# Performance work log

Hardware: AMD Instinct MI355X
Metric: run time of the kernel (lower is better)

The kernel has to match this reference:

```python
import jax, jax.numpy as jnp
import numpy as np

B, T, C, H = 2, 2048, 1024, 16
D = C // H
CURV = 1.0  # clamp_curvature(1.0) -> 1.0
EPS = 1e-5


def layer_norm(x, w, b):
    mu = jnp.mean(x, axis=-1, keepdims=True)
    var = jnp.var(x, axis=-1, keepdims=True)
    return (x - mu) * jax.lax.rsqrt(var + EPS) * w + b


def mobius_addition(x, y, c):
    xn2 = jnp.sum(x * x, axis=-1, keepdims=True)
    yn2 = jnp.sum(y * y, axis=-1, keepdims=True)
    ip = jnp.sum(x * y, axis=-1, keepdims=True)
    num = (1 + 2 * c * ip + c * yn2) * x + (1 - c * xn2) * y
    den = 1 + 2 * c * ip + (c ** 2) * xn2 * yn2
    return num / den


def scaling_factor(x, c):
    xn2 = jnp.sum(x * x, axis=-1, keepdims=True)
    return 2.0 / (1.0 + c * xn2)


def expmap(x, v, c):
    lam = scaling_factor(x, c)
    vn = jnp.linalg.norm(v, axis=-1, keepdims=True)
    second = (1.0 / c ** 0.5) * jnp.tanh(jnp.sqrt(c * lam * vn ** 2 / 2.0)) * v / vn
    return mobius_addition(x, second, c)


def logmap(x, u, c):
    lam = scaling_factor(x, c)
    m = mobius_addition(-x, u, c)
    mn = jnp.linalg.norm(m, axis=-1, keepdims=True)
    cf = 2.0 / (lam * c ** 0.5)
    arg = jnp.clip(jnp.sqrt(c * mn), -0.999, 0.999)
    return cf * jnp.arctanh(arg) * m / mn


def calc_reference_point(x):
    # shift-right by one token, zero at position 0
    return jnp.pad(x[:, :-1, :], ((0, 0), (1, 0), (0, 0)))


def causal_attention(q, k, v):
    # q,k,v: [B,H,T,D]
    scores = jnp.einsum('bhqd,bhkd->bhqk', q, k) / np.sqrt(D).astype(np.float32)
    mask = jnp.tril(jnp.ones((T, T), dtype=bool))
    scores = jnp.where(mask, scores, -jnp.inf)
    att = jax.nn.softmax(scores, axis=-1)
    return jnp.einsum('bhqk,bhkd->bhqd', att, v)


def setup_inputs() -> dict:
    key = jax.random.key(0)
    ks = jax.random.split(key, 6)
    s = 0.02
    return {
        'x': jax.random.normal(ks[0], (B, T, C), jnp.float32),
        'ln1_w': jnp.ones((C,), jnp.float32),
        'ln1_b': jnp.zeros((C,), jnp.float32),
        'W_attn': jax.random.normal(ks[1], (C, 3 * C), jnp.float32) * s,
        'b_attn': jnp.zeros((3 * C,), jnp.float32),
        'W_aproj': jax.random.normal(ks[2], (C, C), jnp.float32) * s,
        'b_aproj': jnp.zeros((C,), jnp.float32),
        'ln2_w': jnp.ones((C,), jnp.float32),
        'ln2_b': jnp.zeros((C,), jnp.float32),
        'W_fc': jax.random.normal(ks[3], (C, 4 * C), jnp.float32) * s,
        'b_fc': jnp.zeros((4 * C,), jnp.float32),
        'W_mproj': jax.random.normal(ks[4], (4 * C, C), jnp.float32) * s,
        'b_mproj': jnp.zeros((C,), jnp.float32),
    }


def reference(x, ln1_w, ln1_b, W_attn, b_attn, W_aproj, b_aproj,
              ln2_w, ln2_b, W_fc, b_fc, W_mproj, b_mproj):
    c = CURV
    # --- attention branch ---
    xn = layer_norm(x, ln1_w, ln1_b)
    ref = calc_reference_point(xn)
    xt = logmap(ref, xn, c)
    qkv = xt @ W_attn + b_attn
    q, k, v = jnp.split(qkv, 3, axis=-1)
    q = q.reshape(B, T, H, D).transpose(0, 2, 1, 3)
    k = k.reshape(B, T, H, D).transpose(0, 2, 1, 3)
    v = v.reshape(B, T, H, D).transpose(0, 2, 1, 3)
    y = causal_attention(q, k, v)
    y = y.transpose(0, 2, 1, 3).reshape(B, T, C)
    y = expmap(ref, y, c)  # map_back_after_attention=True
    y = y @ W_aproj + b_aproj
    x = x + y
    # --- MLP branch (no expmap since map_back_after_attention) ---
    h = layer_norm(x, ln2_w, ln2_b)
    h = jax.nn.gelu(h @ W_fc + b_fc, approximate=False)
    h = h @ W_mproj + b_mproj
    return x + h
```

## Files before the change

kernel.cpp:

```cpp
#include <hip/hip_runtime.h>
#include <hip/hip_bf16.h>
#include <math.h>

#define BDIM 2
#define TSEQ 2048
#define CDIM 1024
#define HNUM 16
#define NROW (BDIM*TSEQ)
#define AST 88

typedef __attribute__((ext_vector_type(8))) short bf16x8_t;
typedef __attribute__((ext_vector_type(4))) float f32x4_t;

__device__ inline float bf2f(__hip_bfloat16 h) { return __bfloat162float(h); }

__device__ inline void unpack8(uint4 u, float* f) {
  unsigned v[4] = {u.x, u.y, u.z, u.w};
  #pragma unroll
  for (int i = 0; i < 4; ++i) {
    union { unsigned u2; float f2; } a, b;
    a.u2 = v[i] << 16;
    b.u2 = v[i] & 0xffff0000u;
    f[2*i]   = a.f2;
    f[2*i+1] = b.f2;
  }
}

__device__ inline void gload16(const void* g, void* l) {
  __builtin_amdgcn_global_load_lds(
      (const __attribute__((address_space(1))) void*)g,
      (__attribute__((address_space(3))) void*)l, 16, 0, 0);
}

__global__ __launch_bounds__(256) void zero32_kernel(float* p, int n) {
  int i = blockIdx.x * 256 + threadIdx.x;
  if (i < n) p[i] = 0.f;
}

__global__ __launch_bounds__(256) void convT_kernel(const float* __restrict__ src,
    __hip_bfloat16* __restrict__ dst, int K, int N)
{
  __shared__ float tile[32][33];
  const int k0 = blockIdx.x * 32, n0 = blockIdx.y * 32;
  const int tr  = threadIdx.x >> 3;
  const int tc4 = (threadIdx.x & 7) * 4;
  float4 v = *(const float4*)(src + (size_t)(k0 + tr) * N + n0 + tc4);
  tile[tr][tc4+0] = v.x; tile[tr][tc4+1] = v.y;
  tile[tr][tc4+2] = v.z; tile[tr][tc4+3] = v.w;
  __syncthreads();
  union { ushort4 u; __hip_bfloat16 h[4]; } o;
  #pragma unroll
  for (int j = 0; j < 4; ++j) o.h[j] = __float2bfloat16(tile[tc4+j][tr]);
  *(ushort4*)(dst + (size_t)(n0 + tr) * K + k0 + tc4) = o.u;
}

__device__ inline void blk_reduce3(float& a, float& b, float& c, float* red) {
  const int lane = threadIdx.x & 63, wv = threadIdx.x >> 6;
  #pragma unroll
  for (int off = 32; off; off >>= 1) {
    a += __shfl_xor(a, off); b += __shfl_xor(b, off); c += __shfl_xor(c, off);
  }
  if (lane == 0) { red[wv] = a; red[4+wv] = b; red[8+wv] = c; }
  __syncthreads();
  a = red[0]+red[1]+red[2]+red[3];
  b = red[4]+red[5]+red[6]+red[7];
  c = red[8]+red[9]+red[10]+red[11];
}

__global__ __launch_bounds__(256) void ln_kernel(const float* __restrict__ x,
    const float* __restrict__ w, const float* __restrict__ b,
    __hip_bfloat16* __restrict__ out)
{
  const int row = blockIdx.x;
  const size_t base = (size_t)row * CDIM;
  const int lane = threadIdx.x & 63, wv = threadIdx.x >> 6;
  float v[4]; float s = 0.f, s2 = 0.f;
  #pragma unroll
  for (int k = 0; k < 4; ++k) {
    int d = threadIdx.x + k*256;
    float xe = x[base + d];
    v[k] = xe; s += xe; s2 += xe*xe;
  }
  __shared__ float red[8];
  #pragma unroll
  for (int off = 32; off; off >>= 1) { s += __shfl_xor(s, off); s2 += __shfl_xor(s2, off); }
  if (lane == 0) { red[wv] = s; red[4+wv] = s2; }
  __syncthreads();
  s  = red[0]+red[1]+red[2]+red[3];
  s2 = red[4]+red[5]+red[6]+red[7];
  float mu = s * (1.0f/CDIM);
  float var = s2 * (1.0f/CDIM) - mu*mu;
  float rstd = rsqrtf(fmaxf(var, 0.f) + 1e-5f);
  #pragma unroll
  for (int k = 0; k < 4; ++k) {
    int d = threadIdx.x + k*256;
    out[base + d] = __float2bfloat16((v[k]-mu)*rstd*w[d] + b[d]);
  }
}

__global__ __launch_bounds__(256) void scalmix1_kernel(const __hip_bfloat16* __restrict__ xn,
                                                       __hip_bfloat16* __restrict__ xt)
{
  const int row = blockIdx.x;
  const bool has = (row & (TSEQ-1)) != 0;
  const __hip_bfloat16* u  = xn + (size_t)row * CDIM;
  const __hip_bfloat16* xp = xn + (size_t)(has ? row-1 : row) * CDIM;
  float ue[4], xe[4];
  float sxx = 0.f, suu = 0.f, sxu = 0.f;
  #pragma unroll
  for (int k = 0; k < 4; ++k) {
    int d = threadIdx.x + k*256;
    ue[k] = bf2f(u[d]);
    xe[k] = has ? bf2f(xp[d]) : 0.f;
    sxx += xe[k]*xe[k]; suu += ue[k]*ue[k]; sxu += xe[k]*ue[k];
  }
  __shared__ float red[12];
  blk_reduce3(sxx, suu, sxu, red);
  float den = 1.f - 2.f*sxu + sxx*suu;
  float inv = 1.f / fmaxf(den, 1e-30f);
  float cb = 1.f - sxx;
  float ca = 1.f - 2.f*sxu + suu;
  float mm = inv*inv*(cb*cb*suu - 2.f*ca*cb*sxu + ca*ca*sxx);
  float mn = sqrtf(fmaxf(mm, 0.f));
  float arg = fminf(sqrtf(mn), 0.999f);
  float fac = (1.f + sxx) * atanhf(arg) / fmaxf(mn, 1e-30f);
  float P = fac*cb*inv;
  float Q = has ? -fac*ca*inv : 0.f;
  #pragma unroll
  for (int k = 0; k < 4; ++k) {
    int d = threadIdx.x + k*256;
    xt[(size_t)row*CDIM + d] = __float2bfloat16(P*ue[k] + Q*xe[k]);
  }
}

__global__ __launch_bounds__(256) void scalmix2_kernel(const __hip_bfloat16* __restrict__ xn,
                                                       const __hip_bfloat16* __restrict__ y,
                                                       __hip_bfloat16* __restrict__ e)
{
  const int row = blockIdx.x;
  const bool has = (row & (TSEQ-1)) != 0;
  const __hip_bfloat16* xp = xn + (size_t)(has ? row-1 : row) * CDIM;
  const __hip_bfloat16* vr = y + (size_t)row * CDIM;
  float ve[4], xe[4];
  float sxx = 0.f, svv = 0.f, sxv = 0.f;
  #pragma unroll
  for (int k = 0; k < 4; ++k) {
    int d = threadIdx.x + k*256;
    ve[k] = bf2f(vr[d]);
    xe[k] = has ? bf2f(xp[d]) : 0.f;
    sxx += xe[k]*xe[k]; svv += ve[k]*ve[k]; sxv += xe[k]*ve[k];
  }
  __shared__ float red[12];
  blk_reduce3(sxx, svv, sxv, red);
  float lam = 2.f / (1.f + sxx);
  float vn  = sqrtf(fmaxf(svv, 1e-30f));
  float th  = tanhf(vn * sqrtf(0.5f*lam));
  float s   = th / vn;
  float yn2 = th*th;
  float ip  = s * sxv;
  float den = 1.f + 2.f*ip + sxx*yn2;
  float inv = 1.f / fmaxf(den, 1e-30f);
  float S = (1.f - sxx)*s*inv;
  float R = has ? (1.f + 2.f*ip + yn2)*inv : 0.f;
  #pragma unroll
  for (int k = 0; k < 4; ++k) {
    int d = threadIdx.x + k*256;
    e[(size_t)row*CDIM + d] = __float2bfloat16(S*ve[k] + R*xe[k]);
  }
}

template<int BM, int BN, int MODE>
__global__ __launch_bounds__(256) void gemmT_kernel(
    const __hip_bfloat16* __restrict__ A, int lda,
    const __hip_bfloat16* __restrict__ Bt, int ldb,
    const float* __restrict__ bias,
    const float* __restrict__ res,
    void* __restrict__ outp,
    int N, int K)
{
  __shared__ __align__(16) __hip_bfloat16 As[2][BM*32];
  __shared__ __align__(16) __hip_bfloat16 Bs[2][BN*32];
  const int bm = blockIdx.x, bn = blockIdx.y;
  const int tid = threadIdx.x, lane = tid & 63, wv = tid >> 6;
  constexpr int FM = BM/32, FN = BN/32;
  const int wm = (wv >> 1) * (BM/2), wn = (wv & 1) * (BN/2);
  f32x4_t acc[FM][FN];
  #pragma unroll
  for (int m = 0; m < FM; ++m)
    #pragma unroll
    for (int n = 0; n < FN; ++n) acc[m][n] = (f32x4_t){0.f,0.f,0.f,0.f};

  const int fr = lane & 15, quad = lane >> 4, q8 = quad * 8;
  const int srow = lane >> 2, scol = (lane & 3) * 8;
  constexpr int SA = BM/16, SB = BN/16;
  const __hip_bfloat16* Ag = A  + (size_t)(bm*BM + srow)*lda + scol;
  const __hip_bfloat16* Bg = Bt + (size_t)(bn*BN + srow)*ldb + scol;

  const int nk = K/32;
  #pragma unroll
  for (int i = 0; i < SA/4; ++i) {
    int s = wv*(SA/4) + i;
    gload16(Ag + (size_t)(s*16)*lda, &As[0][s*512]);
  }
  #pragma unroll
  for (int i = 0; i < SB/4; ++i) {
    int s = wv*(SB/4) + i;
    gload16(Bg + (size_t)(s*16)*ldb, &Bs[0][s*512]);
  }
  __syncthreads();

  int cur = 0;
  for (int t = 0; t < nk; ++t) {
    if (t + 1 < nk) {
      const int k0 = (t+1)*32;
      #pragma unroll
      for (int i = 0; i < SA/4; ++i) {
        int s = wv*(SA/4) + i;
        gload16(Ag + (size_t)(s*16)*lda + k0, &As[cur^1][s*512]);
      }
      #pragma unroll
      for (int i = 0; i < SB/4; ++i) {
        int s = wv*(SB/4) + i;
        gload16(Bg + (size_t)(s*16)*ldb + k0, &Bs[cur^1][s*512]);
      }
    }
    bf16x8_t af[FM], bfr[FN];
    #pragma unroll
    for (int m = 0; m < FM; ++m) af[m]  = *(const bf16x8_t*)&As[cur][(wm + m*16 + fr)*32 + q8];
    #pragma unroll
    for (int n = 0; n < FN; ++n) bfr[n] = *(const bf16x8_t*)&Bs[cur][(wn + n*16 + fr)*32 + q8];
    __builtin_amdgcn_s_setprio(1);
    #pragma unroll
    for (int m = 0; m < FM; ++m)
      #pragma unroll
      for (int n = 0; n < FN; ++n)
        acc[m][n] = __builtin_amdgcn_mfma_f32_16x16x32_bf16(af[m], bfr[n], acc[m][n], 0, 0, 0);
    __builtin_amdgcn_s_setprio(0);
    if (t + 1 < nk) {
      __syncthreads();
      cur ^= 1;
    }
  }

  #pragma unroll
  for (int m = 0; m < FM; ++m)
  #pragma unroll
  for (int n = 0; n < FN; ++n)
  #pragma unroll
  for (int r = 0; r < 4; ++r) {
    int row = bm*BM + wm + m*16 + quad*4 + r;
    int col = bn*BN + wn + n*16 + fr;
    size_t idx = (size_t)row * N + col;
    float v = acc[m][n][r];
    if (MODE == 0) {
      v += bias[col];
      ((__hip_bfloat16*)outp)[idx] = __float2bfloat16(v);
    } else if (MODE == 1) {
      v += bias[col] + res[idx];
      ((float*)outp)[idx] = v;
    } else if (MODE == 2) {
      v += bias[col];
      v = 0.5f * v * (1.0f + erff(v * 0.70710678118654752f));
      ((__hip_bfloat16*)outp)[idx] = __float2bfloat16(v);
    } else {
      v += res[idx];
      ((float*)outp)[idx] = v;
    }
  }
}

__device__ inline __hip_bfloat16* slot_ptr(__hip_bfloat16* p0, __hip_bfloat16* p1, int s) {
  return (s < 2048) ? p0 + (size_t)s*4096 : p1 + (size_t)(s-2048)*4096;
}

__global__ __launch_bounds__(256) void attn_kernel(const __hip_bfloat16* __restrict__ qkv,
                                                   __hip_bfloat16* __restrict__ y,
                                                   __hip_bfloat16* __restrict__ pO0,
                                                   __hip_bfloat16* __restrict__ pO1,
                                                   float2* __restrict__ ml)
{
  const int wid = blockIdx.x;
  int qt, ci;
  if (wid < 32)      { qt = 31 - (wid >> 2); ci = wid & 3; }
  else if (wid < 56) { int w = wid - 32; qt = 23 - w/3; ci = w - (23 - qt)*3; }
  else if (wid < 72) { int w = wid - 56; qt = 15 - (w >> 1); ci = w & 1; }
  else               { qt = 79 - wid; ci = 0; }
  const int tb = ci * 8;
  const int te = min(tb + 8, qt + 1);
  const bool direct = (qt < 8);

  const int pair = blockIdx.y;
  const int b  = pair >> 4;
  const int h  = pair & 15;
  const int tid = threadIdx.x;
  const int lane = tid & 63;
  const int wv = tid >> 6;
  const int t0 = qt * 64;

  __shared__ __align__(16) __hip_bfloat16 Ks[64*AST];
  __shared__ __align__(16) __hip_bfloat16 Vt[64*AST];
  __shared__ __align__(16) __hip_bfloat16 Ps[4][16*AST];

  const int colq = lane & 15, quad = lane >> 4;
  const int q8 = quad * 8;

  const __hip_bfloat16* qp = qkv + ((size_t)(b*TSEQ + t0 + wv*16 + colq))*(3*CDIM) + h*64;
  const bf16x8_t qa0 = *(const bf16x8_t*)(qp + q8);
  const bf16x8_t qa1 = *(const bf16x8_t*)(qp + 32 + q8);

  f32x4_t oacc[4];
  #pragma unroll
  for (int tn = 0; tn < 4; ++tn) oacc[tn] = (f32x4_t){0.f,0.f,0.f,0.f};
  float mr[4] = {-1e30f,-1e30f,-1e30f,-1e30f};
  float lr[4] = {0.f,0.f,0.f,0.f};

  const int jr = tid >> 2;
  const int sg = (tid & 3) * 16;
  const size_t kvbase = ((size_t)(b*TSEQ))*(3*CDIM) + h*64;

  uint4 ck0, ck1, cv0, cv1;
  {
    const __hip_bfloat16* kp = qkv + kvbase + (size_t)(tb*64 + jr)*(3*CDIM) + CDIM + sg;
    ck0 = *(const uint4*)(kp);
    ck1 = *(const uint4*)(kp + 8);
    cv0 = *(const uint4*)(kp + CDIM);
    cv1 = *(const uint4*)(kp + CDIM + 8);
  }
  uint4 nk0 = ck0, nk1 = ck1, nv0 = cv0, nv1 = cv1;

  for (int t = tb; t < te; ++t) {
    __syncthreads();
    {
      *(uint4*)(&Ks[jr*AST + sg])     = ck0;
      *(uint4*)(&Ks[jr*AST + sg + 8]) = ck1;
      union { uint4 u; __hip_bfloat16 hh[8]; } a0, a1;
      a0.u = cv0; a1.u = cv1;
      #pragma unroll
      for (int e = 0; e < 8; ++e) Vt[(sg + e)*AST + jr]     = a0.hh[e];
      #pragma unroll
      for (int e = 0; e < 8; ++e) Vt[(sg + 8 + e)*AST + jr] = a1.hh[e];
    }
    if (t + 1 < te) {
      const __hip_bfloat16* kp = qkv + kvbase + (size_t)((t+1)*64 + jr)*(3*CDIM) + CDIM + sg;
      nk0 = *(const uint4*)(kp);
      nk1 = *(const uint4*)(kp + 8);
      nv0 = *(const uint4*)(kp + CDIM);
      nv1 = *(const uint4*)(kp + CDIM + 8);
    }
    __syncthreads();

    f32x4_t sacc[4];
    __builtin_amdgcn_s_setprio(1);
    #pragma unroll
    for (int tn = 0; tn < 4; ++tn) {
      sacc[tn] = (f32x4_t){0.f,0.f,0.f,0.f};
      bf16x8_t bk0 = *(const bf16x8_t*)(&Ks[(tn*16 + colq)*AST + q8]);
      sacc[tn] = __builtin_amdgcn_mfma_f32_16x16x32_bf16(qa0, bk0, sacc[tn], 0, 0, 0);
      bf16x8_t bk1 = *(const bf16x8_t*)(&Ks[(tn*16 + colq)*AST + 32 + q8]);
      sacc[tn] = __builtin_amdgcn_mfma_f32_16x16x32_bf16(qa1, bk1, sacc[tn], 0, 0, 0);
    }
    __builtin_amdgcn_s_setprio(0);

    float sc[4][4];
    #pragma unroll
    for (int tn = 0; tn < 4; ++tn)
    #pragma unroll
    for (int r = 0; r < 4; ++r) sc[tn][r] = sacc[tn][r] * 0.125f;
    if (t == qt) {
      #pragma unroll
      for (int tn = 0; tn < 4; ++tn)
      #pragma unroll
      for (int r = 0; r < 4; ++r) {
        int key = t*64 + tn*16 + colq;
        int row = t0 + wv*16 + quad*4 + r;
        if (key > row) sc[tn][r] = -1e30f;
      }
    }

    float mx[4];
    #pragma unroll
    for (int r = 0; r < 4; ++r) {
      mx[r] = fmaxf(fmaxf(sc[0][r], sc[1][r]), fmaxf(sc[2][r], sc[3][r]));
      #pragma unroll
      for (int off = 8; off; off >>= 1) mx[r] = fmaxf(mx[r], __shfl_xor(mx[r], off));
    }
    float al[4];
    #pragma unroll
    for (int r = 0; r < 4; ++r) {
      float mn = fmaxf(mr[r], mx[r]);
      al[r] = __expf(mr[r] - mn);
      mr[r] = mn;
    }
    float psum[4] = {0.f,0.f,0.f,0.f};
    #pragma unroll
    for (int tn = 0; tn < 4; ++tn)
    #pragma unroll
    for (int r = 0; r < 4; ++r) {
      float p = __expf(sc[tn][r] - mr[r]);
      psum[r] += p;
      Ps[wv][(quad*4 + r)*AST + tn*16 + colq] = __float2bfloat16(p);
    }
    #pragma unroll
    for (int r = 0; r < 4; ++r) {
      #pragma unroll
      for (int off = 8; off; off >>= 1) psum[r] += __shfl_xor(psum[r], off);
      lr[r] = lr[r]*al[r] + psum[r];
    }
    #pragma unroll
    for (int tn = 0; tn < 4; ++tn)
    #pragma unroll
    for (int r = 0; r < 4; ++r) oacc[tn][r] *= al[r];

    bf16x8_t pa0 = *(const bf16x8_t*)(&Ps[wv][colq*AST + q8]);
    bf16x8_t pa1 = *(const bf16x8_t*)(&Ps[wv][colq*AST + 32 + q8]);
    __builtin_amdgcn_s_setprio(1);
    #pragma unroll
    for (int tn = 0; tn < 4; ++tn) {
      bf16x8_t vb0 = *(const bf16x8_t*)(&Vt[(tn*16 + colq)*AST + q8]);
      oacc[tn] = __builtin_amdgcn_mfma_f32_16x16x32_bf16(pa0, vb0, oacc[tn], 0, 0, 0);
      bf16x8_t vb1 = *(const bf16x8_t*)(&Vt[(tn*16 + colq)*AST + 32 + q8]);
      oacc[tn] = __builtin_amdgcn_mfma_f32_16x16x32_bf16(pa1, vb1, oacc[tn], 0, 0, 0);
    }
    __builtin_amdgcn_s_setprio(0);

    ck0 = nk0; ck1 = nk1; cv0 = nv0; cv1 = nv1;
  }

  if (direct) {
    __hip_bfloat16* yp = y + ((size_t)(b*TSEQ + t0 + wv*16))*CDIM + h*64;
    #pragma unroll
    for (int tn = 0; tn < 4; ++tn)
    #pragma unroll
    for (int r = 0; r < 4; ++r) {
      yp[(size_t)(quad*4 + r)*CDIM + tn*16 + colq] = __float2bfloat16(oacc[tn][r] / lr[r]);
    }
  } else {
    int off = (qt >= 24) ? 40 + (qt-24)*4 : (qt >= 16) ? 16 + (qt-16)*3 : (qt-8)*2;
    int s = pair*72 + off + ci;
    __hip_bfloat16* op = slot_ptr(pO0, pO1, s);
    #pragma unroll
    for (int tn = 0; tn < 4; ++tn)
    #pragma unroll
    for (int r = 0; r < 4; ++r) {
      op[wv*1024 + tn*256 + r*64 + lane] = __float2bfloat16(oacc[tn][r]);
    }
    if (colq == 0) {
      #pragma unroll
      for (int r = 0; r < 4; ++r)
        ml[(size_t)s*64 + wv*16 + quad*4 + r] = make_float2(mr[r], lr[r]);
    }
  }
}

__global__ __launch_bounds__(256) void combine_kernel(__hip_bfloat16* __restrict__ pO0,
                                                      __hip_bfloat16* __restrict__ pO1,
                                                      const float2* __restrict__ ml,
                                                      __hip_bfloat16* __restrict__ y)
{
  const int qt = 8 + blockIdx.x;
  const int pair = blockIdx.y;
  const int b = pair >> 4, h = pair & 15;
  const int nch = (qt >= 24) ? 4 : (qt >= 16) ? 3 : 2;
  const int off = (qt >= 24) ? 40 + (qt-24)*4 : (qt >= 16) ? 16 + (qt-16)*3 : (qt-8)*2;
  const int s0 = pair*72 + off;
  const int tid = threadIdx.x;
  const int q = tid >> 2;
  const int dseg = (tid & 3) * 16;

  float mi[4], li[4];
  float M = -1e30f;
  #pragma unroll
  for (int i = 0; i < 4; ++i) {
    if (i < nch) {
      float2 t = ml[(size_t)(s0+i)*64 + q];
      mi[i] = t.x; li[i] = t.y;
      M = fmaxf(M, t.x);
    }
  }
  float w[4]; float denom = 0.f;
  #pragma unroll
  for (int i = 0; i < 4; ++i) {
    if (i < nch) { w[i] = __expf(mi[i] - M); denom += li[i]*w[i]; }
  }
  const int base = (q >> 4)*1024 + (dseg >> 4)*256 + (q & 3)*64 + ((q >> 2) & 3)*16;
  float acc[16];
  #pragma unroll
  for (int j = 0; j < 16; ++j) acc[j] = 0.f;
  #pragma unroll
  for (int i = 0; i < 4; ++i) {
    if (i < nch) {
      const __hip_bfloat16* op = slot_ptr(pO0, pO1, s0+i) + base;
      uint4 u0 = *(const uint4*)(op);
      uint4 u1 = *(const uint4*)(op + 8);
      float f[16];
      unpack8(u0, f); unpack8(u1, f+8);
      #pragma unroll
      for (int j = 0; j < 16; ++j) acc[j] += w[i]*f[j];
    }
  }
  float inv = 1.f / denom;
  union { uint4 u[2]; __hip_bfloat16 hh[16]; } o;
  #pragma unroll
  for (int j = 0; j < 16; ++j) o.hh[j] = __float2bfloat16(acc[j]*inv);
  __hip_bfloat16* yp = y + ((size_t)(b*TSEQ + qt*64 + q))*CDIM + h*64 + dseg;
  *(uint4*)(yp) = o.u[0];
  *(uint4*)(yp + 8) = o.u[1];
}

extern "C" void kernel_launch(void* const* d_in, const int* in_sizes, int n_in,
                              void* d_out, int out_size, void* d_ws, size_t ws_size,
                              hipStream_t stream)
{
  float* out = (float*)d_out;
  __hip_bfloat16* ybuf = (__hip_bfloat16*)d_out;
  float* x2d = (float*)d_out;
  char* ws = (char*)d_ws;
  const size_t KB = 1024, MB = 1024*1024;

  if (ws_size < 49*MB) {
    zero32_kernel<<<(out_size + 255)/256, 256, 0, stream>>>(out, out_size);
    return;
  }

  const float* x      = (const float*)d_in[0];
  const float* ln1w   = (const float*)d_in[1];
  const float* ln1b   = (const float*)d_in[2];
  const float* Wattn  = (const float*)d_in[3];
  const float* battn  = (const float*)d_in[4];
  const float* Waproj = (const float*)d_in[5];
  const float* baproj = (const float*)d_in[6];
  const float* ln2w   = (const float*)d_in[7];
  const float* ln2b   = (const float*)d_in[8];
  const float* Wfc    = (const float*)d_in[9];
  const float* bfc    = (const float*)d_in[10];
  const float* Wmproj = (const float*)d_in[11];
  const float* bmproj = (const float*)d_in[12];

  __hip_bfloat16* xn   = (__hip_bfloat16*)(ws + 64*KB);
  char* big            = ws + 64*KB + 8*MB;
  __hip_bfloat16* qkv  = (__hip_bfloat16*)big;
  __hip_bfloat16* gbuf = (__hip_bfloat16*)big;
  __hip_bfloat16* ebuf = (__hip_bfloat16*)(big + 16*MB);
  __hip_bfloat16* hbuf = xn;
  char* creg           = ws + 64*KB + 32*MB;
  __hip_bfloat16* cWattnT  = (__hip_bfloat16*)creg;
  __hip_bfloat16* xt       = (__hip_bfloat16*)(creg + 8*MB);
  __hip_bfloat16* cWaprojT = (__hip_bfloat16*)creg;
  __hip_bfloat16* cWfcT    = (__hip_bfloat16*)creg;
  __hip_bfloat16* cWmT     = (__hip_bfloat16*)(creg + 8*MB);
  __hip_bfloat16* pO0      = (__hip_bfloat16*)creg;
  __hip_bfloat16* pO1      = (__hip_bfloat16*)((char*)d_out + 8*MB);
  float2* mlbuf            = (float2*)((char*)d_out + 10*MB);

  convT_kernel<<<dim3(32, 96), 256, 0, stream>>>(Wattn,  cWattnT,  1024, 3072);

  ln_kernel<<<NROW, 256, 0, stream>>>(x, ln1w, ln1b, xn);
  scalmix1_kernel<<<NROW, 256, 0, stream>>>(xn, xt);
  gemmT_kernel<128,128,0><<<dim3(32, 24), 256, 0, stream>>>(
      xt, 1024, cWattnT, 1024, battn, nullptr, qkv, 3072, 1024);
  attn_kernel<<<dim3(80, BDIM*HNUM), 256, 0, stream>>>(qkv, ybuf, pO0, pO1, mlbuf);
  combine_kernel<<<dim3(24, BDIM*HNUM), 256, 0, stream>>>(pO0, pO1, mlbuf, ybuf);
  convT_kernel<<<dim3(32, 32), 256, 0, stream>>>(Waproj, cWaprojT, 1024, 1024);
  scalmix2_kernel<<<NROW, 256, 0, stream>>>(xn, ybuf, ebuf);
  gemmT_kernel<64,128,1><<<dim3(64, 8), 256, 0, stream>>>(
      ebuf, 1024, cWaprojT, 1024, baproj, x, x2d, 1024, 1024);
  convT_kernel<<<dim3(32, 128), 256, 0, stream>>>(Wfc,    cWfcT, 1024, 4096);
  convT_kernel<<<dim3(128, 32), 256, 0, stream>>>(Wmproj, cWmT,  4096, 1024);
  ln_kernel<<<NROW, 256, 0, stream>>>(x2d, ln2w, ln2b, hbuf);
  for (int c = 0; c < 2; ++c) {
    gemmT_kernel<128,128,2><<<dim3(32, 16), 256, 0, stream>>>(
        hbuf, 1024, cWfcT + (size_t)c*2048*1024, 1024, bfc + 2048*c, nullptr, gbuf,
        2048, 1024);
    const __hip_bfloat16* Bc = cWmT + 2048*c;
    if (c == 0) {
      gemmT_kernel<64,128,1><<<dim3(64, 8), 256, 0, stream>>>(
          gbuf, 2048, Bc, 4096, bmproj, x2d, x2d, 1024, 2048);
    } else {
      gemmT_kernel<64,128,7><<<dim3(64, 8), 256, 0, stream>>>(
          gbuf, 2048, Bc, 4096, nullptr, x2d, out, 1024, 2048);
    }
  }
}
```

Baseline: 445.7 us.

## Triple-buffer GEMM loads, skip small softmax rescales, shrink GEMM tiles

The GEMM kernel moves from a double-buffered LDS pipeline to a three-stage pipeline. It issues loads two k-steps ahead and uses explicit vmcnt waits with one barrier per iteration, so global-to-LDS latency overlaps with MFMA work. The flash-attention loop now rescales the running max, sum and accumulators only when some row's max grows by more than 8, which removes per-tile exp and multiply work at the cost of a bounded, unnormalised exponent range. Several GEMM launches switch to smaller 64x64 and 64x128 tiles to put more blocks on the many CUs, trading away some per-block data reuse.

After: 440.4 us (median of 3 runs). No clear change (-1.2%).

```diff
diff --git a/kernel.cpp b/kernel.cpp
--- a/kernel.cpp
+++ b/kernel.cpp
@@ -30,6 +30,10 @@
   __builtin_amdgcn_global_load_lds(
       (const __attribute__((address_space(1))) void*)g,
       (__attribute__((address_space(3))) void*)l, 16, 0, 0);
+}
+
+template<int N> __device__ inline void waitcnt_vm() {
+  asm volatile("s_waitcnt vmcnt(%0)" :: "i"(N) : "memory");
 }
 
 __global__ __launch_bounds__(256) void zero32_kernel(float* p, int n) {
@@ -178,8 +182,8 @@
     void* __restrict__ outp,
     int N, int K)
 {
-  __shared__ __align__(16) __hip_bfloat16 As[2][BM*32];
-  __shared__ __align__(16) __hip_bfloat16 Bs[2][BN*32];
+  __shared__ __align__(16) __hip_bfloat16 As[3][BM*32];
+  __shared__ __align__(16) __hip_bfloat16 Bs[3][BN*32];
   const int bm = blockIdx.x, bn = blockIdx.y;
   const int tid = threadIdx.x, lane = tid & 63, wv = tid >> 6;
   constexpr int FM = BM/32, FN = BN/32;
@@ -193,10 +197,12 @@
   const int fr = lane & 15, quad = lane >> 4, q8 = quad * 8;
   const int srow = lane >> 2, scol = (lane & 3) * 8;
   constexpr int SA = BM/16, SB = BN/16;
+  constexpr int L = SA/4 + SB/4;
   const __hip_bfloat16* Ag = A  + (size_t)(bm*BM + srow)*lda + scol;
   const __hip_bfloat16* Bg = Bt + (size_t)(bn*BN + srow)*ldb + scol;
 
   const int nk = K/32;
+
   #pragma unroll
   for (int i = 0; i < SA/4; ++i) {
     int s = wv*(SA/4) + i;
@@ -207,28 +213,40 @@
     int s = wv*(SB/4) + i;
     gload16(Bg + (size_t)(s*16)*ldb, &Bs[0][s*512]);
   }
-  __syncthreads();
-
-  int cur = 0;
+  #pragma unroll
+  for (int i = 0; i < SA/4; ++i) {
+    int s = wv*(SA/4) + i;
+    gload16(Ag + (size_t)(s*16)*lda + 32, &As[1][s*512]);
+  }
+  #pragma unroll
+  for (int i = 0; i < SB/4; ++i) {
+    int s = wv*(SB/4) + i;
+    gload16(Bg + (size_t)(s*16)*ldb + 32, &Bs[1][s*512]);
+  }
+
+  int b0 = 0, b1 = 1, b2 = 2;
   for (int t = 0; t < nk; ++t) {
-    if (t + 1 < nk) {
-      const int k0 = (t+1)*32;
+    if (t + 1 < nk) waitcnt_vm<L>(); else waitcnt_vm<0>();
+    __builtin_amdgcn_s_barrier();
+    __builtin_amdgcn_sched_barrier(0);
+    if (t + 2 < nk) {
+      const int k0 = (t+2)*32;
       #pragma unroll
       for (int i = 0; i < SA/4; ++i) {
         int s = wv*(SA/4) + i;
-        gload16(Ag + (size_t)(s*16)*lda + k0, &As[cur^1][s*512]);
+        gload16(Ag + (size_t)(s*16)*lda + k0, &As[b2][s*512]);
       }
       #pragma unroll
       for (int i = 0; i < SB/4; ++i) {
         int s = wv*(SB/4) + i;
-        gload16(Bg + (size_t)(s*16)*ldb + k0, &Bs[cur^1][s*512]);
+        gload16(Bg + (size_t)(s*16)*ldb + k0, &Bs[b2][s*512]);
       }
     }
     bf16x8_t af[FM], bfr[FN];
     #pragma unroll
-    for (int m = 0; m < FM; ++m) af[m]  = *(const bf16x8_t*)&As[cur][(wm + m*16 + fr)*32 + q8];
-    #pragma unroll
-    for (int n = 0; n < FN; ++n) bfr[n] = *(const bf16x8_t*)&Bs[cur][(wn + n*16 + fr)*32 + q8];
+    for (int m = 0; m < FM; ++m) af[m]  = *(const bf16x8_t*)&As[b0][(wm + m*16 + fr)*32 + q8];
+    #pragma unroll
+    for (int n = 0; n < FN; ++n) bfr[n] = *(const bf16x8_t*)&Bs[b0][(wn + n*16 + fr)*32 + q8];
     __builtin_amdgcn_s_setprio(1);
     #pragma unroll
     for (int m = 0; m < FM; ++m)
@@ -236,10 +254,7 @@
       for (int n = 0; n < FN; ++n)
         acc[m][n] = __builtin_amdgcn_mfma_f32_16x16x32_bf16(af[m], bfr[n], acc[m][n], 0, 0, 0);
     __builtin_amdgcn_s_setprio(0);
-    if (t + 1 < nk) {
-      __syncthreads();
-      cur ^= 1;
-    }
+    int tmp = b0; b0 = b1; b1 = b2; b2 = tmp;
   }
 
   #pragma unroll
@@ -384,12 +399,18 @@
       #pragma unroll
       for (int off = 8; off; off >>= 1) mx[r] = fmaxf(mx[r], __shfl_xor(mx[r], off));
     }
-    float al[4];
-    #pragma unroll
-    for (int r = 0; r < 4; ++r) {
-      float mn = fmaxf(mr[r], mx[r]);
-      al[r] = __expf(mr[r] - mn);
-      mr[r] = mn;
+    bool grow = (mx[0] > mr[0] + 8.f) || (mx[1] > mr[1] + 8.f) ||
+                (mx[2] > mr[2] + 8.f) || (mx[3] > mr[3] + 8.f);
+    if (__any(grow)) {
+      #pragma unroll
+      for (int r = 0; r < 4; ++r) {
+        float mn = fmaxf(mr[r], mx[r]);
+        float al = __expf(mr[r] - mn);
+        mr[r] = mn;
+        lr[r] *= al;
+        #pragma unroll
+        for (int tn = 0; tn < 4; ++tn) oacc[tn][r] *= al;
+      }
     }
     float psum[4] = {0.f,0.f,0.f,0.f};
     #pragma unroll
@@ -404,12 +425,8 @@
     for (int r = 0; r < 4; ++r) {
       #pragma unroll
       for (int off = 8; off; off >>= 1) psum[r] += __shfl_xor(psum[r], off);
-      lr[r] = lr[r]*al[r] + psum[r];
-    }
-    #pragma unroll
-    for (int tn = 0; tn < 4; ++tn)
-    #pragma unroll
-    for (int r = 0; r < 4; ++r) oacc[tn][r] *= al[r];
+      lr[r] += psum[r];
+    }
 
     bf16x8_t pa0 = *(const bf16x8_t*)(&Ps[wv][colq*AST + q8]);
     bf16x8_t pa1 = *(const bf16x8_t*)(&Ps[wv][colq*AST + 32 + q8]);
@@ -562,21 +579,21 @@
   combine_kernel<<<dim3(24, BDIM*HNUM), 256, 0, stream>>>(pO0, pO1, mlbuf, ybuf);
   convT_kernel<<<dim3(32, 32), 256, 0, stream>>>(Waproj, cWaprojT, 1024, 1024);
   scalmix2_kernel<<<NROW, 256, 0, stream>>>(xn, ybuf, ebuf);
-  gemmT_kernel<64,128,1><<<dim3(64, 8), 256, 0, stream>>>(
+  gemmT_kernel<64,64,1><<<dim3(64, 16), 256, 0, stream>>>(
       ebuf, 1024, cWaprojT, 1024, baproj, x, x2d, 1024, 1024);
   convT_kernel<<<dim3(32, 128), 256, 0, stream>>>(Wfc,    cWfcT, 1024, 4096);
   convT_kernel<<<dim3(128, 32), 256, 0, stream>>>(Wmproj, cWmT,  4096, 1024);
   ln_kernel<<<NROW, 256, 0, stream>>>(x2d, ln2w, ln2b, hbuf);
   for (int c = 0; c < 2; ++c) {
-    gemmT_kernel<128,128,2><<<dim3(32, 16), 256, 0, stream>>>(
+    gemmT_kernel<64,128,2><<<dim3(64, 16), 256, 0, stream>>>(
         hbuf, 1024, cWfcT + (size_t)c*2048*1024, 1024, bfc + 2048*c, nullptr, gbuf,
         2048, 1024);
     const __hip_bfloat16* Bc = cWmT + 2048*c;
     if (c == 0) {
-      gemmT_kernel<64,128,1><<<dim3(64, 8), 256, 0, stream>>>(
+      gemmT_kernel<64,64,1><<<dim3(64, 16), 256, 0, stream>>>(
           gbuf, 2048, Bc, 4096, bmproj, x2d, x2d, 1024, 2048);
     } else {
-      gemmT_kernel<64,128,7><<<dim3(64, 8), 256, 0, stream>>>(
+      gemmT_kernel<64,64,7><<<dim3(64, 16), 256, 0, stream>>>(
           gbuf, 2048, Bc, 4096, nullptr, x2d, out, 1024, 2048);
     }
   }
```
